# Kernel tuning notes

Measured on AMD Instinct MI355X. Metric: run time of the kernel, lower is better.

The kernel has to match this reference:

```python
import jax, jax.numpy as jnp
import numpy as np

B, S, D, H, V, DFF, L, MAXLEN = 256, 64, 1024, 16, 64, 4096, 8, 64
HD = D // H
SCALE = HD ** -0.5
EPS = 1e-5


def _ln(x, g, b):
    m = jnp.mean(x, axis=-1, keepdims=True)
    v = jnp.mean((x - m) ** 2, axis=-1, keepdims=True)
    return (x - m) * jax.lax.rsqrt(v + EPS) * g + b


def setup_inputs() -> dict:
    key = jax.random.key(0)
    ks = jax.random.split(key, 12)
    n = lambda k, shape: jax.random.normal(k, shape, jnp.float32) * 0.02
    return {
        "x": jax.random.randint(ks[0], (B, S), 0, V + 1),
        "step": 0,
        "token_embed": n(ks[1], (V + 1, D)),
        "step_embed": n(ks[2], (MAXLEN, D)),
        "qkv_w": n(ks[3], (L, 3 * D, D)),
        "qkv_b": jnp.zeros((L, 3 * D), jnp.float32),
        "out_w": n(ks[4], (L, D, D)),
        "out_b": jnp.zeros((L, D), jnp.float32),
        "rel_bias": n(ks[5], (L, 2 * MAXLEN - 1)),
        "w1": n(ks[6], (L, DFF, D)),
        "b1": jnp.zeros((L, DFF), jnp.float32),
        "w2": n(ks[7], (L, D, DFF)),
        "b2": jnp.zeros((L, D), jnp.float32),
        "ln1_g": jnp.ones((L, D), jnp.float32),
        "ln1_b": jnp.zeros((L, D), jnp.float32),
        "ln2_g": jnp.ones((L, D), jnp.float32),
        "ln2_b": jnp.zeros((L, D), jnp.float32),
        "lno_g": jnp.ones((D,), jnp.float32),
        "lno_b": jnp.zeros((D,), jnp.float32),
        "pol_w": n(ks[8], (V, D)),
        "pol_b": jnp.zeros((V,), jnp.float32),
        "val_w": n(ks[9], (1, D)),
        "val_b": jnp.zeros((1,), jnp.float32),
    }


def _forward(x, step, token_embed, step_embed, qkv_w, qkv_b, out_w, out_b,
             rel_bias, w1, b1, w2, b2, ln1_g, ln1_b, ln2_g, ln2_b,
             lno_g, lno_b, pol_w, pol_b, val_w, val_b):
    h = token_embed[x]  # [B,S,D]
    step_idx = min(int(step), MAXLEN - 1)
    h = h + step_embed[step_idx][None, None, :]

    pos = jnp.arange(S)
    rel_idx = jnp.clip(pos[:, None] - pos[None, :] + (MAXLEN - 1), 0, 2 * MAXLEN - 2)  # [S,S]

    def layer(h, p):
        qw, qb, ow, ob, rb, w1_, b1_, w2_, b2_, g1, be1, g2, be2 = p
        qkv = h @ qw.T + qb  # [B,S,3D]
        qkv = qkv.reshape(B, S, 3, H, HD).transpose(2, 0, 3, 1, 4)
        q, k, v = qkv[0], qkv[1], qkv[2]  # [B,H,S,HD]
        scores = jnp.einsum('bhqd,bhkd->bhqk', q, k) * SCALE + rb[rel_idx][None, None]
        probs = jax.nn.softmax(scores, axis=-1)
        attn = jnp.einsum('bhqk,bhkd->bhqd', probs, v)  # [B,H,S,HD]
        attn = attn.transpose(0, 2, 1, 3).reshape(B, S, D) @ ow.T + ob
        h = _ln(h + attn, g1, be1)
        ffn = jax.nn.gelu(h @ w1_.T + b1_, approximate=False) @ w2_.T + b2_
        h = _ln(h + ffn, g2, be2)
        return h, None

    h, _ = jax.lax.scan(layer, h, (qkv_w, qkv_b, out_w, out_b, rel_bias,
                                   w1, b1, w2, b2, ln1_g, ln1_b, ln2_g, ln2_b))
    h = _ln(h, lno_g, lno_b)
    pooled = h.mean(axis=1)  # [B,D]
    policy = pooled @ pol_w.T + pol_b  # [B,V]
    value = pooled @ val_w.T + val_b   # [B,1]
    return policy, value, h


def reference(x, step, token_embed, step_embed, qkv_w, qkv_b, out_w, out_b,
              rel_bias, w1, b1, w2, b2, ln1_g, ln1_b, ln2_g, ln2_b,
              lno_g, lno_b, pol_w, pol_b, val_w, val_b):
    return _forward(x, step, token_embed, step_embed, qkv_w, qkv_b, out_w, out_b,
                    rel_bias, w1, b1, w2, b2, ln1_g, ln1_b, ln2_g, ln2_b,
                    lno_g, lno_b, pol_w, pol_b, val_w, val_b)
```

## Files before the change

### kernel.cpp

```cpp
#include <hip/hip_runtime.h>
#include <math.h>

typedef _Float16 f16;
typedef _Float16 f16x8 __attribute__((ext_vector_type(8)));
typedef _Float16 f16x4 __attribute__((ext_vector_type(4)));
typedef float floatx4 __attribute__((ext_vector_type(4)));

#define BATCH 256
#define SEQ 64
#define DMODEL 1024
#define NHEAD 16
#define HDIM 64
#define VOCAB 64
#define DFF 4096
#define NLAYER 8
#define MS (BATCH*SEQ)

#define GPTR(p) ((const __attribute__((address_space(1))) void*)(p))
#define LPTR(p) ((__attribute__((address_space(3))) void*)(p))

__device__ __forceinline__ floatx4 mfma16(f16x8 a, f16x8 b, floatx4 c) {
    return __builtin_amdgcn_mfma_f32_16x16x32_f16(a, b, c, 0, 0, 0);
}

__device__ __forceinline__ float gelu_f(float x) {
    return 0.5f * x * (1.f + erff(x * 0.70710678118654752f));
}

__global__ __launch_bounds__(256) void embed_k(const int* __restrict__ x, const int* __restrict__ step,
                                               const float* __restrict__ tok, const float* __restrict__ se,
                                               f16* __restrict__ r) {
    int row = blockIdx.x;
    int t = threadIdx.x;
    int id = x[row];
    int si = min(max(step[0], 0), 63);
    float4 a = ((const float4*)(tok + (size_t)id * DMODEL))[t];
    float4 b = ((const float4*)(se + (size_t)si * DMODEL))[t];
    f16x4 hv; hv[0] = (f16)(a.x + b.x); hv[1] = (f16)(a.y + b.y);
    hv[2] = (f16)(a.z + b.z); hv[3] = (f16)(a.w + b.w);
    ((f16x4*)(r + (size_t)row * DMODEL))[t] = hv;
}

__global__ __launch_bounds__(256) void cvt4_k(const float* __restrict__ qw, const float* __restrict__ ow,
                                              const float* __restrict__ w1, const float* __restrict__ w2,
                                              f16* __restrict__ dq, f16* __restrict__ dO,
                                              f16* __restrict__ d1, f16* __restrict__ d2) {
    int gid = blockIdx.x * 256 + threadIdx.x;
    const float4* s; f16x4* d; int off;
    if (gid < 786432)        { s = (const float4*)qw; d = (f16x4*)dq; off = gid; }
    else if (gid < 1048576)  { s = (const float4*)ow; d = (f16x4*)dO; off = gid - 786432; }
    else if (gid < 2097152)  { s = (const float4*)w1; d = (f16x4*)d1; off = gid - 1048576; }
    else                     { s = (const float4*)w2; d = (f16x4*)d2; off = gid - 2097152; }
    float4 v = s[off];
    f16x4 o; o[0] = (f16)v.x; o[1] = (f16)v.y; o[2] = (f16)v.z; o[3] = (f16)v.w;
    d[off] = o;
}

template<int MODE>
__global__ __launch_bounds__(256, 2) void gemm_k(const f16* __restrict__ A, const f16* __restrict__ Bw,
                                                 const float* __restrict__ bias,
                                                 f16* __restrict__ Cb,
                                                 const f16* __restrict__ Rres, f16* __restrict__ ResOut,
                                                 float2* __restrict__ Part,
                                                 int M, int N, int K) {
    __shared__ f16 smem[32768];

    const int tid = threadIdx.x;
    const int lane = tid & 63;
    const int wave = tid >> 6;
    const int wm = wave >> 1, wn = wave & 1;
    const int lr = lane & 15, lg = lane >> 4;
    const int sa = lr & 7;

    const unsigned nx = gridDim.x;
    const unsigned nwg = nx * gridDim.y;
    unsigned flat = blockIdx.y * nx + blockIdx.x;
    flat = (flat & 7u) * (nwg >> 3) + (flat >> 3);
    const int m0 = (int)(flat / nx) * 128;
    const int n0 = (int)(flat % nx) * 128;

    floatx4 acc[4][4] = {};

    const int srow = tid >> 3;
    const int scbs = (tid & 7) ^ (srow & 7);
    const f16* Asrc = A + (size_t)(m0 + srow) * K + scbs * 8;
    const f16* Bsrc = Bw + (size_t)(n0 + srow) * K + scbs * 8;
    const int ldsw = wave * 512;

#define STAGE(bi, tt) do {                                                                        \
    const f16* _a = Asrc + (size_t)(tt) * 64;                                                     \
    const f16* _b = Bsrc + (size_t)(tt) * 64;                                                     \
    f16* _l = smem + ((bi) << 14) + ldsw;                                                         \
    __builtin_amdgcn_global_load_lds(GPTR(_a),                  LPTR(_l),         16, 0, 0);      \
    __builtin_amdgcn_global_load_lds(GPTR(_a + 32 * (size_t)K), LPTR(_l + 2048),  16, 0, 0);      \
    __builtin_amdgcn_global_load_lds(GPTR(_a + 64 * (size_t)K), LPTR(_l + 4096),  16, 0, 0);      \
    __builtin_amdgcn_global_load_lds(GPTR(_a + 96 * (size_t)K), LPTR(_l + 6144),  16, 0, 0);      \
    __builtin_amdgcn_global_load_lds(GPTR(_b),                  LPTR(_l + 8192),  16, 0, 0);      \
    __builtin_amdgcn_global_load_lds(GPTR(_b + 32 * (size_t)K), LPTR(_l + 10240), 16, 0, 0);      \
    __builtin_amdgcn_global_load_lds(GPTR(_b + 64 * (size_t)K), LPTR(_l + 12288), 16, 0, 0);      \
    __builtin_amdgcn_global_load_lds(GPTR(_b + 96 * (size_t)K), LPTR(_l + 14336), 16, 0, 0);      \
} while (0)

#define TILE_BODY(t_, bi) do {                                                                    \
    if ((t_) + 1 < NT) STAGE((bi) ^ 1, (t_) + 1);                                                 \
    const f16* Ab = smem + ((bi) << 14);                                                          \
    const f16* Bb = Ab + 8192;                                                                    \
    f16x8 af[8], bf[8];                                                                           \
    _Pragma("unroll") for (int kh = 0; kh < 2; ++kh)                                              \
    _Pragma("unroll") for (int mi = 0; mi < 4; ++mi)                                              \
        af[kh * 4 + mi] = *(const f16x8*)(Ab + (wm * 64 + mi * 16 + lr) * 64                      \
                                          + (((kh * 4 + lg) ^ sa) << 3));                         \
    _Pragma("unroll") for (int kh = 0; kh < 2; ++kh)                                              \
    _Pragma("unroll") for (int ni = 0; ni < 4; ++ni)                                              \
        bf[kh * 4 + ni] = *(const f16x8*)(Bb + (wn * 64 + ni * 16 + lr) * 64                      \
                                          + (((kh * 4 + lg) ^ sa) << 3));                         \
    __builtin_amdgcn_s_setprio(1);                                                                \
    _Pragma("unroll") for (int kh = 0; kh < 2; ++kh)                                              \
    _Pragma("unroll") for (int mi = 0; mi < 4; ++mi)                                              \
    _Pragma("unroll") for (int ni = 0; ni < 4; ++ni)                                              \
        acc[mi][ni] = mfma16(af[kh * 4 + mi], bf[kh * 4 + ni], acc[mi][ni]);                      \
    __builtin_amdgcn_s_setprio(0);                                                                \
    if ((t_) + 1 < NT) { asm volatile("s_waitcnt vmcnt(0)" ::: "memory"); }                       \
    __builtin_amdgcn_s_barrier();                                                                 \
} while (0)

    const int NT = K >> 6;

    STAGE(0, 0);
    asm volatile("s_waitcnt vmcnt(0)" ::: "memory");
    __builtin_amdgcn_s_barrier();

    for (int t = 0; t < NT; t += 2) {
        TILE_BODY(t, 0);
        TILE_BODY(t + 1, 1);
    }
#undef STAGE
#undef TILE_BODY

    if (MODE == 2) {
        float bsv[4];
#pragma unroll
        for (int ni = 0; ni < 4; ++ni) bsv[ni] = bias[n0 + wn * 64 + ni * 16 + lr];
        f16* scr = smem + wave * 4096;
#pragma unroll
        for (int mi = 0; mi < 4; ++mi)
#pragma unroll
            for (int ni = 0; ni < 4; ++ni)
#pragma unroll
                for (int j = 0; j < 4; ++j) {
                    int rr = mi * 16 + lg * 4 + j;
                    int cc = ni * 16 + lr;
                    scr[rr * 64 + (((cc >> 3) ^ (rr & 7)) * 8) + (cc & 7)]
                        = (f16)(acc[mi][ni][j] + bsv[ni]);
                }
        int gr = m0 + wm * 64 + lane;
        const f16* rrow = Rres + (size_t)gr * N + n0 + wn * 64;
        f16* orow = ResOut + (size_t)gr * N + n0 + wn * 64;
        float s = 0.f, ss = 0.f;
#pragma unroll
        for (int i = 0; i < 8; ++i) {
            f16x8 a = *(const f16x8*)(scr + lane * 64 + ((i ^ (lane & 7)) * 8));
            f16x8 rv = *(const f16x8*)(rrow + i * 8);
            f16x8 o;
#pragma unroll
            for (int k = 0; k < 8; ++k) {
                float v = (float)a[k] + (float)rv[k];
                s += v; ss += v * v;
                o[k] = (f16)v;
            }
            *(f16x8*)(orow + i * 8) = o;
        }
        float* red = (float*)(smem + 16384);
        if (wn == 1) { red[(wm * 64 + lane) * 2] = s; red[(wm * 64 + lane) * 2 + 1] = ss; }
        __syncthreads();
        if (wn == 0) {
            float s2 = red[(wm * 64 + lane) * 2], ss2 = red[(wm * 64 + lane) * 2 + 1];
            Part[(size_t)gr * (N >> 7) + (n0 >> 7)] = float2{s + s2, ss + ss2};
        }
    } else {
        f16* scr = smem + wave * 4096;
        float bsv[4];
#pragma unroll
        for (int ni = 0; ni < 4; ++ni) bsv[ni] = bias[n0 + wn * 64 + ni * 16 + lr];
#pragma unroll
        for (int mi = 0; mi < 4; ++mi)
#pragma unroll
            for (int ni = 0; ni < 4; ++ni)
#pragma unroll
                for (int j = 0; j < 4; ++j) {
                    int rr = mi * 16 + lg * 4 + j;
                    int cc = ni * 16 + lr;
                    float v = acc[mi][ni][j] + bsv[ni];
                    if (MODE == 1) v = gelu_f(v);
                    scr[rr * 64 + (((cc >> 3) ^ (rr & 7)) * 8) + (cc & 7)] = (f16)v;
                }
        int gr = m0 + wm * 64 + lane;
        f16* dst = Cb + (size_t)gr * N + n0 + wn * 64;
#pragma unroll
        for (int i = 0; i < 8; ++i) {
            f16x8 v = *(const f16x8*)(scr + lane * 64 + ((i ^ (lane & 7)) * 8));
            *(f16x8*)(dst + i * 8) = v;
        }
    }
}

__global__ __launch_bounds__(64) void attn_k(const f16* __restrict__ qkv, const float* __restrict__ rb,
                                             f16* __restrict__ ctx) {
    const int hh = blockIdx.x;
    const int bb = blockIdx.y;
    const int lane = threadIdx.x;
    __shared__ float rbs[128];
    __shared__ f16 Vt[64][72];
    __shared__ f16 Pl[64][72];

    for (int i = lane; i < 127; i += 64) rbs[i] = rb[i];

    const f16* vrow = qkv + (size_t)(bb * 64 + lane) * 3072 + 2048 + hh * 64;
#pragma unroll
    for (int i = 0; i < 8; ++i) {
        f16x8 v = *(const f16x8*)(vrow + i * 8);
#pragma unroll
        for (int j = 0; j < 8; ++j) Vt[i * 8 + j][lane] = v[j];
    }
    __syncthreads();

    const int lr = lane & 15, lg = lane >> 4;
    floatx4 sacc[4][4] = {};
    const f16* qbase = qkv + (size_t)(bb * 64) * 3072 + hh * 64;
#pragma unroll
    for (int kk = 0; kk < 64; kk += 32) {
        f16x8 qa[4], kb[4];
#pragma unroll
        for (int mf = 0; mf < 4; ++mf)
            qa[mf] = *(const f16x8*)(qbase + (size_t)(mf * 16 + lr) * 3072 + kk + lg * 8);
#pragma unroll
        for (int nf = 0; nf < 4; ++nf)
            kb[nf] = *(const f16x8*)(qbase + 1024 + (size_t)(nf * 16 + lr) * 3072 + kk + lg * 8);
#pragma unroll
        for (int mf = 0; mf < 4; ++mf)
#pragma unroll
            for (int nf = 0; nf < 4; ++nf)
                sacc[mf][nf] = mfma16(qa[mf], kb[nf], sacc[mf][nf]);
    }

#pragma unroll
    for (int mf = 0; mf < 4; ++mf) {
#pragma unroll
        for (int j = 0; j < 4; ++j) {
            int qrow = mf * 16 + lg * 4 + j;
            float v0 = sacc[mf][0][j] * 0.125f + rbs[qrow - (0  + lr) + 63];
            float v1 = sacc[mf][1][j] * 0.125f + rbs[qrow - (16 + lr) + 63];
            float v2 = sacc[mf][2][j] * 0.125f + rbs[qrow - (32 + lr) + 63];
            float v3 = sacc[mf][3][j] * 0.125f + rbs[qrow - (48 + lr) + 63];
            float mx = fmaxf(fmaxf(v0, v1), fmaxf(v2, v3));
            for (int m = 1; m < 16; m <<= 1) mx = fmaxf(mx, __shfl_xor(mx, m));
            v0 = __expf(v0 - mx); v1 = __expf(v1 - mx); v2 = __expf(v2 - mx); v3 = __expf(v3 - mx);
            float sum = v0 + v1 + v2 + v3;
            for (int m = 1; m < 16; m <<= 1) sum += __shfl_xor(sum, m);
            float inv = 1.f / sum;
            Pl[qrow][0  + lr] = (f16)(v0 * inv);
            Pl[qrow][16 + lr] = (f16)(v1 * inv);
            Pl[qrow][32 + lr] = (f16)(v2 * inv);
            Pl[qrow][48 + lr] = (f16)(v3 * inv);
        }
    }
    __syncthreads();

    floatx4 oacc[4][4] = {};
#pragma unroll
    for (int kk = 0; kk < 64; kk += 32) {
        f16x8 pa[4], vb[4];
#pragma unroll
        for (int mf = 0; mf < 4; ++mf) pa[mf] = *(const f16x8*)&Pl[mf * 16 + lr][kk + lg * 8];
#pragma unroll
        for (int nf = 0; nf < 4; ++nf) vb[nf] = *(const f16x8*)&Vt[nf * 16 + lr][kk + lg * 8];
#pragma unroll
        for (int mf = 0; mf < 4; ++mf)
#pragma unroll
            for (int nf = 0; nf < 4; ++nf)
                oacc[mf][nf] = mfma16(pa[mf], vb[nf], oacc[mf][nf]);
    }
    __syncthreads();
#pragma unroll
    for (int mf = 0; mf < 4; ++mf)
#pragma unroll
        for (int nf = 0; nf < 4; ++nf)
#pragma unroll
            for (int j = 0; j < 4; ++j)
                Pl[mf * 16 + lg * 4 + j][nf * 16 + lr] = (f16)oacc[mf][nf][j];
    __syncthreads();
    f16* crow = ctx + (size_t)(bb * 64 + lane) * DMODEL + hh * 64;
#pragma unroll
    for (int i = 0; i < 8; ++i) {
        f16x8 v = *(const f16x8*)&Pl[lane][i * 8];
        *(f16x8*)(crow + i * 8) = v;
    }
}

__global__ __launch_bounds__(128) void ln_k(const f16* __restrict__ res, const float2* __restrict__ part,
                                            const float* __restrict__ g, const float* __restrict__ b,
                                            f16* __restrict__ out) {
    int row = blockIdx.x;
    int t = threadIdx.x;
    f16x8 rv = ((const f16x8*)(res + (size_t)row * DMODEL))[t];
    float s = 0.f, ss = 0.f;
#pragma unroll
    for (int c = 0; c < 8; ++c) {
        float2 p = part[(size_t)row * 8 + c];
        s += p.x; ss += p.y;
    }
    float mean = s * (1.f / 1024.f);
    float var = ss * (1.f / 1024.f) - mean * mean;
    float rstd = rsqrtf(var + 1e-5f);
    float4 g0 = ((const float4*)g)[t * 2], g1 = ((const float4*)g)[t * 2 + 1];
    float4 b0 = ((const float4*)b)[t * 2], b1 = ((const float4*)b)[t * 2 + 1];
    f16x8 o;
    o[0] = (f16)(((float)rv[0] - mean) * rstd * g0.x + b0.x);
    o[1] = (f16)(((float)rv[1] - mean) * rstd * g0.y + b0.y);
    o[2] = (f16)(((float)rv[2] - mean) * rstd * g0.z + b0.z);
    o[3] = (f16)(((float)rv[3] - mean) * rstd * g0.w + b0.w);
    o[4] = (f16)(((float)rv[4] - mean) * rstd * g1.x + b1.x);
    o[5] = (f16)(((float)rv[5] - mean) * rstd * g1.y + b1.y);
    o[6] = (f16)(((float)rv[6] - mean) * rstd * g1.z + b1.z);
    o[7] = (f16)(((float)rv[7] - mean) * rstd * g1.w + b1.w);
    ((f16x8*)(out + (size_t)row * DMODEL))[t] = o;
}

__global__ __launch_bounds__(256) void lnf_k(const f16* __restrict__ res, const float* __restrict__ g,
                                             const float* __restrict__ b, float* __restrict__ h) {
    int row = blockIdx.x;
    int t = threadIdx.x;
    f16x4 rv = ((const f16x4*)(res + (size_t)row * DMODEL))[t];
    float v0 = (float)rv[0], v1 = (float)rv[1], v2 = (float)rv[2], v3 = (float)rv[3];
    float s = v0 + v1 + v2 + v3;
    float ss = v0 * v0 + v1 * v1 + v2 * v2 + v3 * v3;
    for (int m = 1; m < 64; m <<= 1) { s += __shfl_xor(s, m); ss += __shfl_xor(ss, m); }
    __shared__ float red[8];
    if ((t & 63) == 0) { red[(t >> 6) * 2] = s; red[(t >> 6) * 2 + 1] = ss; }
    __syncthreads();
    s = red[0] + red[2] + red[4] + red[6];
    ss = red[1] + red[3] + red[5] + red[7];
    float mean = s * (1.f / 1024.f);
    float var = ss * (1.f / 1024.f) - mean * mean;
    float rstd = rsqrtf(var + 1e-5f);
    float4 gg = ((const float4*)g)[t];
    float4 bb = ((const float4*)b)[t];
    float4 o;
    o.x = (v0 - mean) * rstd * gg.x + bb.x;
    o.y = (v1 - mean) * rstd * gg.y + bb.y;
    o.z = (v2 - mean) * rstd * gg.z + bb.z;
    o.w = (v3 - mean) * rstd * gg.w + bb.w;
    ((float4*)(h + (size_t)row * DMODEL))[t] = o;
}

__global__ __launch_bounds__(256) void pool_k(const float* __restrict__ h, float* __restrict__ pooled) {
    int b = blockIdx.x;
    int t = threadIdx.x;
    float sx = 0, sy = 0, sz = 0, sw = 0;
    for (int s = 0; s < SEQ; ++s) {
        float4 v = ((const float4*)(h + (size_t)(b * SEQ + s) * DMODEL))[t];
        sx += v.x; sy += v.y; sz += v.z; sw += v.w;
    }
    float4 o; o.x = sx * (1.f / 64.f); o.y = sy * (1.f / 64.f); o.z = sz * (1.f / 64.f); o.w = sw * (1.f / 64.f);
    ((float4*)(pooled + (size_t)b * DMODEL))[t] = o;
}

__global__ __launch_bounds__(64) void head_k(const float* __restrict__ pooled, const float* __restrict__ pw,
                                             const float* __restrict__ pb, const float* __restrict__ vw,
                                             const float* __restrict__ vb, float* __restrict__ out) {
    int b = blockIdx.x;
    int lane = threadIdx.x;
    const float* pr = pooled + (size_t)b * DMODEL;
    const float* wr = pw + (size_t)lane * DMODEL;
    float accp = 0.f;
    for (int d = 0; d < DMODEL; d += 4) {
        float4 x = *(const float4*)(pr + d);
        float4 w = *(const float4*)(wr + d);
        accp += x.x * w.x + x.y * w.y + x.z * w.z + x.w * w.w;
    }
    float accv = 0.f;
    for (int d = lane * 4; d < DMODEL; d += 256) {
        float4 x = *(const float4*)(pr + d);
        float4 w = *(const float4*)(vw + d);
        accv += x.x * w.x + x.y * w.y + x.z * w.z + x.w * w.w;
    }
    for (int m = 1; m < 64; m <<= 1) accv += __shfl_xor(accv, m);
    out[b * VOCAB + lane] = accp + pb[lane];
    if (lane == 0) out[BATCH * VOCAB + b] = accv + vb[0];
}

extern "C" void kernel_launch(void* const* d_in, const int* in_sizes, int n_in,
                              void* d_out, int out_size, void* d_ws, size_t ws_size,
                              hipStream_t stream) {
    const int*   x      = (const int*)d_in[0];
    const int*   step   = (const int*)d_in[1];
    const float* tok    = (const float*)d_in[2];
    const float* se     = (const float*)d_in[3];
    const float* qkv_w  = (const float*)d_in[4];
    const float* qkv_b  = (const float*)d_in[5];
    const float* out_w  = (const float*)d_in[6];
    const float* out_b  = (const float*)d_in[7];
    const float* relb   = (const float*)d_in[8];
    const float* w1     = (const float*)d_in[9];
    const float* b1     = (const float*)d_in[10];
    const float* w2     = (const float*)d_in[11];
    const float* b2     = (const float*)d_in[12];
    const float* ln1g   = (const float*)d_in[13];
    const float* ln1b   = (const float*)d_in[14];
    const float* ln2g   = (const float*)d_in[15];
    const float* ln2b   = (const float*)d_in[16];
    const float* lnog   = (const float*)d_in[17];
    const float* lnob   = (const float*)d_in[18];
    const float* pw     = (const float*)d_in[19];
    const float* pb     = (const float*)d_in[20];
    const float* vw     = (const float*)d_in[21];
    const float* vb     = (const float*)d_in[22];

    float* out = (float*)d_out;
    float* h = out + BATCH * VOCAB + BATCH;

    char* ws = (char*)d_ws;
    f16* rB     = (f16*)(ws);
    f16* resA   = (f16*)(ws + 33554432);
    f16* qkv16  = (f16*)(ws + 67108864);
    f16* ctx16  = (f16*)(ws + 167772160);
    f16* ffn16  = (f16*)(ws + 67108864);
    f16* wqb    = (f16*)(ws + 201326592);
    f16* wob    = (f16*)(ws + 207618048);
    f16* w1b    = (f16*)(ws + 209715200);
    f16* w2b    = (f16*)(ws + 218103808);
    float2* part = (float2*)(ws + 226492416);
    float* pooled = (float*)(ws + 226492416);

    embed_k<<<MS, 256, 0, stream>>>(x, step, tok, se, rB);

    for (int l = 0; l < NLAYER; ++l) {
        cvt4_k<<<12288, 256, 0, stream>>>(qkv_w + (size_t)l * 3145728, out_w + (size_t)l * 1048576,
                                          w1 + (size_t)l * 4194304, w2 + (size_t)l * 4194304,
                                          wqb, wob, w1b, w2b);

        gemm_k<0><<<dim3(24, 128), 256, 0, stream>>>(rB, wqb, qkv_b + l * 3072, qkv16,
                                                     nullptr, nullptr, nullptr, MS, 3072, 1024);
        attn_k<<<dim3(NHEAD, BATCH), 64, 0, stream>>>(qkv16, relb + l * 127, ctx16);
        gemm_k<2><<<dim3(8, 128), 256, 0, stream>>>(ctx16, wob, out_b + l * 1024, nullptr,
                                                    rB, resA, part, MS, 1024, 1024);
        ln_k<<<MS, 128, 0, stream>>>(resA, part, ln1g + l * 1024, ln1b + l * 1024, rB);
        gemm_k<1><<<dim3(32, 128), 256, 0, stream>>>(rB, w1b, b1 + l * 4096, ffn16,
                                                     nullptr, nullptr, nullptr, MS, 4096, 1024);
        gemm_k<2><<<dim3(8, 128), 256, 0, stream>>>(ffn16, w2b, b2 + l * 1024, nullptr,
                                                    rB, resA, part, MS, 1024, 4096);
        ln_k<<<MS, 128, 0, stream>>>(resA, part, ln2g + l * 1024, ln2b + l * 1024, rB);
    }

    lnf_k<<<MS, 256, 0, stream>>>(rB, lnog, lnob, h);
    pool_k<<<BATCH, 256, 0, stream>>>(h, pooled);
    head_k<<<BATCH, 64, 0, stream>>>(pooled, pw, pb, vw, vb, out);
}
```

Before: 5.012 ms.

## Triple-buffer B tiles with two-ahead prefetch and use sigmoid-form tanh GELU

Splits GEMM LDS staging into separate A and B buffers, keeping A double-buffered while B is triple-buffered and prefetched two K-tiles ahead. Partial vmcnt waits replace full drains, so loads stay in flight across iterations. GELU switches from erf to the tanh approximation expressed via exp. This raises LDS use per block and slightly changes the activation's numerics.

```diff
diff --git a/kernel.cpp b/kernel.cpp
--- a/kernel.cpp
+++ b/kernel.cpp
@@ -24,7 +24,9 @@
 }
 
 __device__ __forceinline__ float gelu_f(float x) {
-    return 0.5f * x * (1.f + erff(x * 0.70710678118654752f));
+    float x3 = x * x * x;
+    float y = -1.5957691216f * fmaf(0.044715f, x3, x);
+    return x / (1.f + __expf(y));
 }
 
 __global__ __launch_bounds__(256) void embed_k(const int* __restrict__ x, const int* __restrict__ step,
@@ -63,7 +65,7 @@
                                                  const f16* __restrict__ Rres, f16* __restrict__ ResOut,
                                                  float2* __restrict__ Part,
                                                  int M, int N, int K) {
-    __shared__ f16 smem[32768];
+    __shared__ f16 smem[40960];
 
     const int tid = threadIdx.x;
     const int lane = tid & 63;
@@ -87,55 +89,72 @@
     const f16* Bsrc = Bw + (size_t)(n0 + srow) * K + scbs * 8;
     const int ldsw = wave * 512;
 
-#define STAGE(bi, tt) do {                                                                        \
+#define STAGEA(bi, tt) do {                                                                       \
     const f16* _a = Asrc + (size_t)(tt) * 64;                                                     \
+    f16* _l = smem + (bi) * 8192 + ldsw;                                                          \
+    __builtin_amdgcn_global_load_lds(GPTR(_a),                  LPTR(_l),        16, 0, 0);       \
+    __builtin_amdgcn_global_load_lds(GPTR(_a + 32 * (size_t)K), LPTR(_l + 2048), 16, 0, 0);       \
+    __builtin_amdgcn_global_load_lds(GPTR(_a + 64 * (size_t)K), LPTR(_l + 4096), 16, 0, 0);       \
+    __builtin_amdgcn_global_load_lds(GPTR(_a + 96 * (size_t)K), LPTR(_l + 6144), 16, 0, 0);       \
+} while (0)
+
+#define STAGEB(bi, tt) do {                                                                       \
     const f16* _b = Bsrc + (size_t)(tt) * 64;                                                     \
-    f16* _l = smem + ((bi) << 14) + ldsw;                                                         \
-    __builtin_amdgcn_global_load_lds(GPTR(_a),                  LPTR(_l),         16, 0, 0);      \
-    __builtin_amdgcn_global_load_lds(GPTR(_a + 32 * (size_t)K), LPTR(_l + 2048),  16, 0, 0);      \
-    __builtin_amdgcn_global_load_lds(GPTR(_a + 64 * (size_t)K), LPTR(_l + 4096),  16, 0, 0);      \
-    __builtin_amdgcn_global_load_lds(GPTR(_a + 96 * (size_t)K), LPTR(_l + 6144),  16, 0, 0);      \
-    __builtin_amdgcn_global_load_lds(GPTR(_b),                  LPTR(_l + 8192),  16, 0, 0);      \
-    __builtin_amdgcn_global_load_lds(GPTR(_b + 32 * (size_t)K), LPTR(_l + 10240), 16, 0, 0);      \
-    __builtin_amdgcn_global_load_lds(GPTR(_b + 64 * (size_t)K), LPTR(_l + 12288), 16, 0, 0);      \
-    __builtin_amdgcn_global_load_lds(GPTR(_b + 96 * (size_t)K), LPTR(_l + 14336), 16, 0, 0);      \
+    f16* _l = smem + 16384 + (bi) * 8192 + ldsw;                                                  \
+    __builtin_amdgcn_global_load_lds(GPTR(_b),                  LPTR(_l),        16, 0, 0);       \
+    __builtin_amdgcn_global_load_lds(GPTR(_b + 32 * (size_t)K), LPTR(_l + 2048), 16, 0, 0);       \
+    __builtin_amdgcn_global_load_lds(GPTR(_b + 64 * (size_t)K), LPTR(_l + 4096), 16, 0, 0);       \
+    __builtin_amdgcn_global_load_lds(GPTR(_b + 96 * (size_t)K), LPTR(_l + 6144), 16, 0, 0);       \
 } while (0)
 
-#define TILE_BODY(t_, bi) do {                                                                    \
-    if ((t_) + 1 < NT) STAGE((bi) ^ 1, (t_) + 1);                                                 \
-    const f16* Ab = smem + ((bi) << 14);                                                          \
-    const f16* Bb = Ab + 8192;                                                                    \
-    f16x8 af[8], bf[8];                                                                           \
-    _Pragma("unroll") for (int kh = 0; kh < 2; ++kh)                                              \
-    _Pragma("unroll") for (int mi = 0; mi < 4; ++mi)                                              \
-        af[kh * 4 + mi] = *(const f16x8*)(Ab + (wm * 64 + mi * 16 + lr) * 64                      \
-                                          + (((kh * 4 + lg) ^ sa) << 3));                         \
-    _Pragma("unroll") for (int kh = 0; kh < 2; ++kh)                                              \
-    _Pragma("unroll") for (int ni = 0; ni < 4; ++ni)                                              \
-        bf[kh * 4 + ni] = *(const f16x8*)(Bb + (wn * 64 + ni * 16 + lr) * 64                      \
-                                          + (((kh * 4 + lg) ^ sa) << 3));                         \
-    __builtin_amdgcn_s_setprio(1);                                                                \
-    _Pragma("unroll") for (int kh = 0; kh < 2; ++kh)                                              \
-    _Pragma("unroll") for (int mi = 0; mi < 4; ++mi)                                              \
-    _Pragma("unroll") for (int ni = 0; ni < 4; ++ni)                                              \
-        acc[mi][ni] = mfma16(af[kh * 4 + mi], bf[kh * 4 + ni], acc[mi][ni]);                      \
-    __builtin_amdgcn_s_setprio(0);                                                                \
-    if ((t_) + 1 < NT) { asm volatile("s_waitcnt vmcnt(0)" ::: "memory"); }                       \
-    __builtin_amdgcn_s_barrier();                                                                 \
-} while (0)
-
     const int NT = K >> 6;
 
-    STAGE(0, 0);
-    asm volatile("s_waitcnt vmcnt(0)" ::: "memory");
+    STAGEA(0, 0);
+    STAGEB(0, 0);
+    STAGEB(1, 1);
+    asm volatile("s_waitcnt vmcnt(4)" ::: "memory");
     __builtin_amdgcn_s_barrier();
 
-    for (int t = 0; t < NT; t += 2) {
-        TILE_BODY(t, 0);
-        TILE_BODY(t + 1, 1);
-    }
-#undef STAGE
-#undef TILE_BODY
+    int ab = 0, bb = 0;
+    for (int t = 0; t < NT; ++t) {
+        if (t + 1 < NT) STAGEA(ab ^ 1, t + 1);
+        if (t + 2 < NT) { int b2 = bb + 2; if (b2 >= 3) b2 -= 3; STAGEB(b2, t + 2); }
+
+        const f16* Ab = smem + ab * 8192;
+        const f16* Bb = smem + 16384 + bb * 8192;
+        f16x8 af[8], bf[8];
+#pragma unroll
+        for (int kh = 0; kh < 2; ++kh)
+#pragma unroll
+            for (int mi = 0; mi < 4; ++mi)
+                af[kh * 4 + mi] = *(const f16x8*)(Ab + (wm * 64 + mi * 16 + lr) * 64
+                                                  + (((kh * 4 + lg) ^ sa) << 3));
+#pragma unroll
+        for (int kh = 0; kh < 2; ++kh)
+#pragma unroll
+            for (int ni = 0; ni < 4; ++ni)
+                bf[kh * 4 + ni] = *(const f16x8*)(Bb + (wn * 64 + ni * 16 + lr) * 64
+                                                  + (((kh * 4 + lg) ^ sa) << 3));
+
+        __builtin_amdgcn_s_setprio(1);
+#pragma unroll
+        for (int kh = 0; kh < 2; ++kh)
+#pragma unroll
+            for (int mi = 0; mi < 4; ++mi)
+#pragma unroll
+                for (int ni = 0; ni < 4; ++ni)
+                    acc[mi][ni] = mfma16(af[kh * 4 + mi], bf[kh * 4 + ni], acc[mi][ni]);
+        __builtin_amdgcn_s_setprio(0);
+
+        if (t + 2 < NT)      { asm volatile("s_waitcnt vmcnt(4)" ::: "memory"); }
+        else if (t + 1 < NT) { asm volatile("s_waitcnt vmcnt(0)" ::: "memory"); }
+        __builtin_amdgcn_s_barrier();
+
+        ab ^= 1;
+        bb = (bb == 2) ? 0 : bb + 1;
+    }
+#undef STAGEA
+#undef STAGEB
 
     if (MODE == 2) {
         float bsv[4];
```

Measured after the change: 4.920 ms. About the same (-1.8%).
